# Kernel tuning notes

Hardware: AMD Instinct MI355X
Metric: run time of the kernel (lower is better)

## Reference

```python
import jax, jax.numpy as jnp
import numpy as np

B, N, DIM, QK_DIM, HEADS, GS, M = 4, 8000, 256, 128, 8, 128, 256


def setup_inputs() -> dict:
    key = jax.random.key(0)
    ks = jax.random.split(key, 8)
    normed_x = jax.random.normal(ks[0], (B, N, DIM), jnp.float32)
    # idx_last is a per-batch permutation (token reordering index), shape [B, N, 1]
    idx_last = jax.vmap(lambda k: jax.random.permutation(k, N))(
        jax.random.split(ks[1], B)).astype(jnp.int32)[..., None]
    k_global = jax.random.normal(ks[2], (HEADS, M, QK_DIM // HEADS), jnp.float32)
    v_global = jax.random.normal(ks[3], (HEADS, M, DIM // HEADS), jnp.float32)
    s = 1.0 / np.sqrt(DIM).astype(np.float32)
    Wq = jax.random.normal(ks[4], (QK_DIM, DIM), jnp.float32) * s
    Wk = jax.random.normal(ks[5], (QK_DIM, DIM), jnp.float32) * s
    Wv = jax.random.normal(ks[6], (DIM, DIM), jnp.float32) * s
    Wp = jax.random.normal(ks[7], (DIM, DIM), jnp.float32) * s
    return {"normed_x": normed_x, "idx_last": idx_last, "k_global": k_global,
            "v_global": v_global, "Wq": Wq, "Wk": Wk, "Wv": Wv, "Wp": Wp}


def _forward(normed_x, idx_last, k_global, v_global, Wq, Wk, Wv, Wp):
    x = normed_x
    b, n, _ = x.shape
    h = HEADS
    idx = idx_last[..., 0]  # [B, N]

    q = x @ Wq.T  # [B, N, QK_DIM]
    k = x @ Wk.T  # [B, N, QK_DIM]
    v = x @ Wv.T  # [B, N, DIM]

    # reorder tokens (gather along the token axis)
    q = jnp.take_along_axis(q, idx[:, :, None], axis=1)
    k = jnp.take_along_axis(k, idx[:, :, None], axis=1)
    v = jnp.take_along_axis(v, idx[:, :, None], axis=1)

    gs = min(n, GS)
    ng = (n + gs - 1) // gs
    pad_n = ng * gs - n

    # pad queries by reflecting the tail, then split into ng groups of gs
    pq = jnp.concatenate([q, jnp.flip(q[:, n - pad_n:n], axis=1)], axis=1)
    pq = pq.reshape(b, ng, gs, h, -1).transpose(0, 1, 3, 2, 4)  # b ng h gs dq

    # keys/values padded with an extra gs of reflected tail -> overlapping windows
    kr = jnp.concatenate([k, jnp.flip(k[:, n - pad_n - gs:n], axis=1)], axis=1)
    vr = jnp.concatenate([v, jnp.flip(v[:, n - pad_n - gs:n], axis=1)], axis=1)
    k_win = jnp.concatenate([kr[:, :ng * gs].reshape(b, ng, gs, -1),
                             kr[:, gs:].reshape(b, ng, gs, -1)], axis=2)
    v_win = jnp.concatenate([vr[:, :ng * gs].reshape(b, ng, gs, -1),
                             vr[:, gs:].reshape(b, ng, gs, -1)], axis=2)
    pk = k_win.reshape(b, ng, 2 * gs, h, -1).transpose(0, 1, 3, 2, 4)  # b ng h 2gs dq
    pv = v_win.reshape(b, ng, 2 * gs, h, -1).transpose(0, 1, 3, 2, 4)  # b ng h 2gs dv

    scale = pq.shape[-1] ** (-0.5)

    # local overlapping-window attention
    s1 = jnp.einsum('bghqd,bghkd->bghqk', pq, pk) * scale
    o1 = jnp.einsum('bghqk,bghkd->bghqd', jax.nn.softmax(s1, axis=-1), pv)

    # global attention (k_global/v_global broadcast over batch and groups)
    s2 = jnp.einsum('bghqd,hmd->bghqm', pq, k_global) * scale
    o2 = jnp.einsum('bghqm,hmd->bghqd', jax.nn.softmax(s2, axis=-1), v_global)

    out = (o1 + o2).transpose(0, 1, 3, 2, 4).reshape(b, ng * gs, -1)[:, :n]

    # scatter back to original token order: res[b, idx[b, i]] = out[b, i]
    b_idx = jnp.arange(b)[:, None]
    out = out.at[b_idx, idx].set(out)
    return out @ Wp.T


def reference(normed_x, idx_last, k_global, v_global, Wq, Wk, Wv, Wp):
    return _forward(normed_x, idx_last, k_global, v_global, Wq, Wk, Wv, Wp)
```

## Files before the change

kernel.cpp:

```cpp
#include <hip/hip_runtime.h>

typedef __attribute__((ext_vector_type(8))) short short8;
typedef __attribute__((ext_vector_type(4))) short short4v;
typedef __attribute__((ext_vector_type(4))) float f32x4;
typedef unsigned short ushort_t;

#define MFMA_BF16_K32(A,B,C) __builtin_amdgcn_mfma_f32_16x16x32_bf16(A,B,C,0,0,0)
#define MFMA_BF16_K16(A,B,C) __builtin_amdgcn_mfma_f32_16x16x16bf16_1k(A,B,C,0,0,0)

static constexpr int Bc  = 4;
static constexpr int Nn  = 8000;
static constexpr int N2  = 8192;
static constexpr int DIMc = 256;
static constexpr float SC2 = 0.36067376022224085f;

__device__ __forceinline__ unsigned short f2bf(float f){
  unsigned int u = __float_as_uint(f);
  u = (u + 0x7FFFu + ((u >> 16) & 1u)) >> 16;
  return (unsigned short)u;
}
__device__ __forceinline__ uint2 pack4(f32x4 v){
  uint2 r;
  r.x = (unsigned)f2bf(v[0]) | ((unsigned)f2bf(v[1]) << 16);
  r.y = (unsigned)f2bf(v[2]) | ((unsigned)f2bf(v[3]) << 16);
  return r;
}
__device__ __forceinline__ unsigned cvtpk(float lo, float hi){
  unsigned r;
  asm("v_cvt_pk_bf16_f32 %0, %1, %2" : "=v"(r) : "v"(lo), "v"(hi));
  return r;
}
__device__ __forceinline__ float rexp2(float x){
  float r;
  asm("v_exp_f32 %0, %1" : "=v"(r) : "v"(x));
  return r;
}
__device__ __forceinline__ float bfhi(unsigned u){ return __uint_as_float(u & 0xffff0000u); }
__device__ __forceinline__ float bflo(unsigned u){ return __uint_as_float(u << 16); }
__device__ __forceinline__ int vperm(int t){
  return (t & ~31) | (((t >> 2) & 3) * 8 + ((t >> 4) & 1) * 4 + (t & 3));
}

__global__ __launch_bounds__(256) void prep_kernel(
    const float* __restrict__ Wq, const float* __restrict__ Wk,
    const float* __restrict__ Wv, const float* __restrict__ Wp,
    const float* __restrict__ kg, const float* __restrict__ vg,
    ushort_t* __restrict__ Wc, ushort_t* __restrict__ vgT,
    ushort_t* __restrict__ kgb, ushort_t* __restrict__ Wpb)
{
  int i = blockIdx.x * 256 + threadIdx.x;
  if (i < 131072){
    int r = i >> 8, c = i & 255;
    float v;
    if (r < 128)      v = Wq[r * 256 + c] * SC2;
    else if (r < 256) v = Wk[(r - 128) * 256 + c];
    else              v = Wv[(r - 256) * 256 + c];
    Wc[i] = f2bf(v);
  } else if (i < 196608){
    int j = i - 131072;
    int c = j & 31, m = (j >> 5) & 255, h = j >> 13;
    vgT[(h * 32 + c) * 256 + vperm(m)] = f2bf(vg[j]);
  } else if (i < 229376){
    int j = i - 196608;
    kgb[j] = f2bf(kg[j]);
  } else {
    int j = i - 229376;
    Wpb[j] = f2bf(Wp[j]);
  }
}

__global__ __launch_bounds__(256) void proj_kernel(
    const float* __restrict__ X, const ushort_t* __restrict__ Wc,
    const int* __restrict__ idx, ushort_t* __restrict__ qh,
    ushort_t* __restrict__ kh, ushort_t* __restrict__ vT)
{
  const int b  = blockIdx.y;
  const int r0 = blockIdx.x * 64;
  const int tid = threadIdx.x;
  const int w = tid >> 6, l = tid & 63, g4 = l >> 4, q16 = l & 15;
  __shared__ unsigned Xs[64][132];

  #pragma unroll
  for (int r = 0; r < 16; ++r){
    int row = r * 4 + w;
    int tok = idx[b * Nn + r0 + row];
    float4 xv = reinterpret_cast<const float4*>(X + (size_t)(b * Nn + tok) * DIMc)[l];
    uint2 u; u.x = cvtpk(xv.x, xv.y); u.y = cvtpk(xv.z, xv.w);
    *reinterpret_cast<uint2*>(&Xs[row][l * 2]) = u;
  }
  __syncthreads();

  f32x4 acc[4][8];
  #pragma unroll
  for (int mt = 0; mt < 4; ++mt)
    #pragma unroll
    for (int ct = 0; ct < 8; ++ct) acc[mt][ct] = f32x4{0.f, 0.f, 0.f, 0.f};
  const int colbase = w * 128;
  #pragma unroll
  for (int kc = 0; kc < 8; ++kc){
    short8 a[4];
    #pragma unroll
    for (int mt = 0; mt < 4; ++mt){
      uint4 au = *reinterpret_cast<const uint4*>(&Xs[mt * 16 + q16][kc * 16 + g4 * 4]);
      a[mt] = __builtin_bit_cast(short8, au);
    }
    #pragma unroll
    for (int ct = 0; ct < 8; ++ct){
      int col = colbase + ct * 16 + q16;
      short8 bb = *reinterpret_cast<const short8*>(Wc + col * 256 + kc * 32 + g4 * 8);
      #pragma unroll
      for (int mt = 0; mt < 4; ++mt) acc[mt][ct] = MFMA_BF16_K32(a[mt], bb, acc[mt][ct]);
    }
  }
  if (w < 2){
    ushort_t* dst = (w == 0) ? qh : kh;
    #pragma unroll
    for (int ct = 0; ct < 8; ++ct){
      #pragma unroll
      for (int mt = 0; mt < 4; ++mt){
        #pragma unroll
        for (int r = 0; r < 4; ++r){
          int j = r0 + mt * 16 + g4 * 4 + r;
          dst[((size_t)(b * 8 + ct) * N2 + j) * 16 + q16] = f2bf(acc[mt][ct][r]);
        }
      }
    }
  } else {
    #pragma unroll
    for (int ct = 0; ct < 8; ++ct){
      int col = colbase - 256 + ct * 16 + q16;
      #pragma unroll
      for (int mt = 0; mt < 4; ++mt){
        int jb = r0 + (mt >> 1) * 32 + g4 * 8 + (mt & 1) * 4;
        *reinterpret_cast<uint2*>(vT + (size_t)(b * 256 + col) * N2 + jb) = pack4(acc[mt][ct]);
      }
    }
  }
}

__global__ __launch_bounds__(256) void reflect_fill_kernel(
    ushort_t* __restrict__ qh, ushort_t* __restrict__ kh, ushort_t* __restrict__ vT)
{
  int t = blockIdx.x * 256 + threadIdx.x;
  if (t < 24576){
    int e = t & 1;
    int r = (t >> 1) % 192;
    int p = (t >> 1) / 192;
    int b = p >> 4, q = p & 15;
    ushort_t* base = (q < 8) ? qh : kh;
    int h = q & 7;
    size_t plane = (size_t)(b * 8 + h) * N2 * 16;
    const uint4* src = reinterpret_cast<const uint4*>(base + plane + (size_t)(7999 - r) * 16);
    uint4*       dst = reinterpret_cast<uint4*>(base + plane + (size_t)(8000 + r) * 16);
    dst[e] = src[e];
  } else {
    int u = t - 24576;
    int r = u / 192, i2 = u % 192;
    vT[(size_t)r * N2 + vperm(8000 + i2)] = vT[(size_t)r * N2 + vperm(7999 - i2)];
  }
}

__global__ __launch_bounds__(256) void attn_kernel(
    const ushort_t* __restrict__ qh, const ushort_t* __restrict__ kh,
    const ushort_t* __restrict__ vT,
    const ushort_t* __restrict__ kg, const ushort_t* __restrict__ vgT,
    ushort_t* __restrict__ aoh)
{
  const int go = blockIdx.x, hp = blockIdx.y, b = blockIdx.z;
  const int tid = threadIdx.x;
  const int w = tid >> 6, l = tid & 63, g4 = l >> 4, q16 = l & 15;
  const int h = hp * 4 + w;
  __shared__ unsigned Pex[4][8][16][17];
  const f32x4 z4 = {0.f, 0.f, 0.f, 0.f};
  const size_t bh = (size_t)(b * 8 + h);
  const ushort_t* Kloc = kh + (bh * N2 + go * 128) * 16;
  const ushort_t* Vloc = vT + (size_t)(b * 256 + h * 32) * N2 + go * 128;
  const ushort_t* Kg   = kg + (size_t)h * 256 * 16;
  const ushort_t* Vg   = vgT + (size_t)h * 32 * 256;
  const ushort_t* Qb   = qh + (bh * N2 + go * 128) * 16;
  ushort_t*       Ob   = aoh + (bh * N2 + go * 128) * 32;

  short8 ones;
  #pragma unroll
  for (int j = 0; j < 8; ++j) ones[j] = (short)0x3F80;

  #pragma unroll 1
  for (int pass = 0; pass < 2; ++pass){
    const ushort_t* kbase = (pass == 0) ? Kloc : Kg;
    short4v karr[16];
    #pragma unroll
    for (int t = 0; t < 16; ++t)
      karr[t] = *reinterpret_cast<const short4v*>(
          kbase + (size_t)(t * 16 + q16) * 16 + g4 * 4);
    const ushort_t* v0;
    size_t rstride;
    if (pass == 0){ v0 = Vloc + (size_t)q16 * N2 + g4 * 8;  rstride = (size_t)16 * N2; }
    else          { v0 = Vg   + (size_t)q16 * 256 + g4 * 8; rstride = (size_t)16 * 256; }
    uint4 va[8], vb[8];
    #pragma unroll
    for (int t2 = 0; t2 < 8; ++t2){
      va[t2] = *reinterpret_cast<const uint4*>(v0 + t2 * 32);
      vb[t2] = *reinterpret_cast<const uint4*>(v0 + rstride + t2 * 32);
    }

    #pragma unroll 2
    for (int qt = 0; qt < 8; ++qt){
      short4v qf = *reinterpret_cast<const short4v*>(
          Qb + (size_t)(qt * 16 + q16) * 16 + g4 * 4);
      f32x4 s[16];
      __builtin_amdgcn_s_setprio(1);
      #pragma unroll
      for (int t = 0; t < 16; ++t) s[t] = MFMA_BF16_K16(karr[t], qf, z4);
      __builtin_amdgcn_s_setprio(0);
      uint4 p4[8];
      #pragma unroll
      for (int t2 = 0; t2 < 8; ++t2){
        float e0 = rexp2(s[2*t2][0]);
        float e1 = rexp2(s[2*t2][1]);
        float e2 = rexp2(s[2*t2][2]);
        float e3 = rexp2(s[2*t2][3]);
        float f0 = rexp2(s[2*t2+1][0]);
        float f1 = rexp2(s[2*t2+1][1]);
        float f2 = rexp2(s[2*t2+1][2]);
        float f3 = rexp2(s[2*t2+1][3]);
        p4[t2].x = cvtpk(e0, e1); p4[t2].y = cvtpk(e2, e3);
        p4[t2].z = cvtpk(f0, f1); p4[t2].w = cvtpk(f2, f3);
      }
      f32x4 o0 = z4, o1 = z4, dacc = z4;
      __builtin_amdgcn_s_setprio(1);
      #pragma unroll
      for (int t2 = 0; t2 < 8; ++t2){
        short8 pf = __builtin_bit_cast(short8, p4[t2]);
        o0   = MFMA_BF16_K32(__builtin_bit_cast(short8, va[t2]), pf, o0);
        o1   = MFMA_BF16_K32(__builtin_bit_cast(short8, vb[t2]), pf, o1);
        dacc = MFMA_BF16_K32(ones, pf, dacc);
      }
      __builtin_amdgcn_s_setprio(0);
      float invd = 1.0f / dacc[0];
      unsigned* pb = &Pex[w][qt][q16][0];
      if (pass == 0){
        pb[g4 * 2]         = cvtpk(o0[0] * invd, o0[1] * invd);
        pb[g4 * 2 + 1]     = cvtpk(o0[2] * invd, o0[3] * invd);
        pb[8 + g4 * 2]     = cvtpk(o1[0] * invd, o1[1] * invd);
        pb[8 + g4 * 2 + 1] = cvtpk(o1[2] * invd, o1[3] * invd);
      } else {
        unsigned u0 = pb[g4 * 2],     u1 = pb[g4 * 2 + 1];
        unsigned u2 = pb[8 + g4 * 2], u3 = pb[8 + g4 * 2 + 1];
        f32x4 r0, r1;
        r0[0] = __builtin_fmaf(o0[0], invd, bflo(u0));
        r0[1] = __builtin_fmaf(o0[1], invd, bfhi(u0));
        r0[2] = __builtin_fmaf(o0[2], invd, bflo(u1));
        r0[3] = __builtin_fmaf(o0[3], invd, bfhi(u1));
        r1[0] = __builtin_fmaf(o1[0], invd, bflo(u2));
        r1[1] = __builtin_fmaf(o1[1], invd, bfhi(u2));
        r1[2] = __builtin_fmaf(o1[2], invd, bflo(u3));
        r1[3] = __builtin_fmaf(o1[3], invd, bfhi(u3));
        uint2 s0, s1;
        s0.x = cvtpk(r0[0], r0[1]); s0.y = cvtpk(r0[2], r0[3]);
        s1.x = cvtpk(r1[0], r1[1]); s1.y = cvtpk(r1[2], r1[3]);
        size_t base = (size_t)(qt * 16 + q16) * 32;
        *reinterpret_cast<uint2*>(Ob + base + g4 * 4)      = s0;
        *reinterpret_cast<uint2*>(Ob + base + 16 + g4 * 4) = s1;
      }
    }
  }
}

__global__ __launch_bounds__(256) void final_kernel(
    const ushort_t* __restrict__ A, const ushort_t* __restrict__ Wp,
    const int* __restrict__ idx, float* __restrict__ out)
{
  const int b  = blockIdx.y;
  const int r0 = blockIdx.x * 64;
  const int tid = threadIdx.x;
  const int w = tid >> 6, l = tid & 63, g4 = l >> 4, q16 = l & 15;
  f32x4 acc[4][4];
  #pragma unroll
  for (int mt = 0; mt < 4; ++mt)
    #pragma unroll
    for (int ct = 0; ct < 4; ++ct) acc[mt][ct] = f32x4{0.f, 0.f, 0.f, 0.f};
  const int colbase = w * 64;
  #pragma unroll
  for (int kc = 0; kc < 8; ++kc){
    short8 a[4];
    #pragma unroll
    for (int mt = 0; mt < 4; ++mt)
      a[mt] = *reinterpret_cast<const short8*>(
          A + ((size_t)(b * 8 + kc) * N2 + r0 + mt * 16 + q16) * 32 + g4 * 8);
    #pragma unroll
    for (int ct = 0; ct < 4; ++ct){
      int col = colbase + ct * 16 + q16;
      short8 bb = *reinterpret_cast<const short8*>(Wp + col * 256 + kc * 32 + g4 * 8);
      #pragma unroll
      for (int mt = 0; mt < 4; ++mt) acc[mt][ct] = MFMA_BF16_K32(a[mt], bb, acc[mt][ct]);
    }
  }
  #pragma unroll
  for (int mt = 0; mt < 4; ++mt){
    int orow[4];
    #pragma unroll
    for (int r = 0; r < 4; ++r) orow[r] = idx[b * Nn + r0 + mt * 16 + g4 * 4 + r];
    #pragma unroll
    for (int ct = 0; ct < 4; ++ct){
      int col = colbase + ct * 16 + q16;
      #pragma unroll
      for (int r = 0; r < 4; ++r)
        out[(size_t)(b * Nn + orow[r]) * DIMc + col] = acc[mt][ct][r];
    }
  }
}

extern "C" void kernel_launch(void* const* d_in, const int* in_sizes, int n_in,
                              void* d_out, int out_size, void* d_ws, size_t ws_size,
                              hipStream_t stream)
{
  const float* x   = (const float*)d_in[0];
  const int*   idx = (const int*)d_in[1];
  const float* kg  = (const float*)d_in[2];
  const float* vg  = (const float*)d_in[3];
  const float* Wq  = (const float*)d_in[4];
  const float* Wk  = (const float*)d_in[5];
  const float* Wv  = (const float*)d_in[6];
  const float* Wp  = (const float*)d_in[7];
  float* out = (float*)d_out;

  char* ws = (char*)d_ws;
  size_t off = 0;
  auto alloc = [&](size_t bytes) -> void* {
    void* p = ws + off; off += (bytes + 255) & ~(size_t)255; return p;
  };
  ushort_t* qh   = (ushort_t*)alloc((size_t)Bc * 8 * N2 * 16 * 2);
  ushort_t* kh   = (ushort_t*)alloc((size_t)Bc * 8 * N2 * 16 * 2);
  ushort_t* vT   = (ushort_t*)alloc((size_t)Bc * 256 * N2 * 2);
  ushort_t* aoh  = (ushort_t*)alloc((size_t)Bc * 8 * N2 * 32 * 2);
  ushort_t* Wc   = (ushort_t*)alloc((size_t)512 * 256 * 2);
  ushort_t* vgT  = (ushort_t*)alloc((size_t)8 * 32 * 256 * 2);
  ushort_t* kgb  = (ushort_t*)alloc((size_t)8 * 256 * 16 * 2);
  ushort_t* Wpb  = (ushort_t*)alloc((size_t)256 * 256 * 2);

  hipLaunchKernelGGL(prep_kernel,  dim3(1152), dim3(256), 0, stream,
                     Wq, Wk, Wv, Wp, kg, vg, Wc, vgT, kgb, Wpb);
  hipLaunchKernelGGL(proj_kernel,  dim3(125, 4), dim3(256), 0, stream, x, Wc, idx, qh, kh, vT);
  hipLaunchKernelGGL(reflect_fill_kernel, dim3(864), dim3(256), 0, stream, qh, kh, vT);
  hipLaunchKernelGGL(attn_kernel,  dim3(63, 2, 4), dim3(256), 0, stream, qh, kh, vT, kgb, vgT, aoh);
  hipLaunchKernelGGL(final_kernel, dim3(125, 4), dim3(256), 0, stream, aoh, Wpb, idx, out);
}
```

Before: 100.8 us.

## Pre-swizzle weights and V into MFMA fragment order for coalesced loads

Weights for the projection and output GEMMs are rearranged in the prep kernel into per-lane MFMA fragment order, so each lane loads one contiguous 16-byte chunk. Local and global V are also stored in a fragment-major layout indexed by group, head and lane, which replaces strided transposed reads in the attention kernel with contiguous ones. The goal is to cut uncoalesced global traffic and address arithmetic. In exchange the V stores in the projection and the reflect fill become scattered, with more complex indexing.

```diff
diff --git a/kernel.cpp b/kernel.cpp
--- a/kernel.cpp
+++ b/kernel.cpp
@@ -40,39 +40,54 @@
 __device__ __forceinline__ int vperm(int t){
   return (t & ~31) | (((t >> 2) & 3) * 8 + ((t >> 4) & 1) * 4 + (t & 3));
 }
+__device__ __forceinline__ size_t vf_addr(int b, int p, int h, int half, int q16v){
+  int g = p >> 7, t2 = (p >> 5) & 3, g4 = (p >> 3) & 3, j = p & 7;
+  return ((size_t)((((b * 64 + g) * 8 + h) * 2 + half) * 4 + t2) * 64
+          + g4 * 16 + q16v) * 8 + j;
+}
 
 __global__ __launch_bounds__(256) void prep_kernel(
     const float* __restrict__ Wq, const float* __restrict__ Wk,
     const float* __restrict__ Wv, const float* __restrict__ Wp,
     const float* __restrict__ kg, const float* __restrict__ vg,
-    ushort_t* __restrict__ Wc, ushort_t* __restrict__ vgT,
-    ushort_t* __restrict__ kgb, ushort_t* __restrict__ Wpb)
+    ushort_t* __restrict__ Wcs, ushort_t* __restrict__ Wps,
+    ushort_t* __restrict__ Vgf, ushort_t* __restrict__ kgb)
 {
   int i = blockIdx.x * 256 + threadIdx.x;
   if (i < 131072){
-    int r = i >> 8, c = i & 255;
+    int jj = i & 7, f = i >> 3;
+    int l = f & 63, kc = (f >> 6) & 7, ctw = f >> 9;
+    int col = ctw * 16 + (l & 15);
+    int k   = kc * 32 + (l >> 4) * 8 + jj;
     float v;
-    if (r < 128)      v = Wq[r * 256 + c] * SC2;
-    else if (r < 256) v = Wk[(r - 128) * 256 + c];
-    else              v = Wv[(r - 256) * 256 + c];
-    Wc[i] = f2bf(v);
+    if (col < 128)      v = Wq[col * 256 + k] * SC2;
+    else if (col < 256) v = Wk[(col - 128) * 256 + k];
+    else                v = Wv[(col - 256) * 256 + k];
+    Wcs[i] = f2bf(v);
   } else if (i < 196608){
-    int j = i - 131072;
-    int c = j & 31, m = (j >> 5) & 255, h = j >> 13;
-    vgT[(h * 32 + c) * 256 + vperm(m)] = f2bf(vg[j]);
-  } else if (i < 229376){
-    int j = i - 196608;
+    int o = i - 131072;
+    int jj = o & 7, f = o >> 3;
+    int l = f & 63, kc = (f >> 6) & 7, ctw = f >> 9;
+    int col = ctw * 16 + (l & 15);
+    int k   = kc * 32 + (l >> 4) * 8 + jj;
+    Wps[o] = f2bf(Wp[col * 256 + k]);
+  } else if (i < 262144){
+    int o = i - 196608;
+    int c = o & 31, m = (o >> 5) & 255, h = o >> 13;
+    int p = vperm(m);
+    int t2 = p >> 5, g4 = (p >> 3) & 3, j = p & 7;
+    int half = c >> 4, q16v = c & 15;
+    Vgf[((size_t)((h * 2 + half) * 8 + t2) * 64 + g4 * 16 + q16v) * 8 + j] = f2bf(vg[o]);
+  } else {
+    int j = i - 262144;
     kgb[j] = f2bf(kg[j]);
-  } else {
-    int j = i - 229376;
-    Wpb[j] = f2bf(Wp[j]);
   }
 }
 
 __global__ __launch_bounds__(256) void proj_kernel(
-    const float* __restrict__ X, const ushort_t* __restrict__ Wc,
+    const float* __restrict__ X, const ushort_t* __restrict__ Wcs,
     const int* __restrict__ idx, ushort_t* __restrict__ qh,
-    ushort_t* __restrict__ kh, ushort_t* __restrict__ vT)
+    ushort_t* __restrict__ kh, ushort_t* __restrict__ Vf)
 {
   const int b  = blockIdx.y;
   const int r0 = blockIdx.x * 64;
@@ -95,7 +110,6 @@
   for (int mt = 0; mt < 4; ++mt)
     #pragma unroll
     for (int ct = 0; ct < 8; ++ct) acc[mt][ct] = f32x4{0.f, 0.f, 0.f, 0.f};
-  const int colbase = w * 128;
   #pragma unroll
   for (int kc = 0; kc < 8; ++kc){
     short8 a[4];
@@ -106,8 +120,8 @@
     }
     #pragma unroll
     for (int ct = 0; ct < 8; ++ct){
-      int col = colbase + ct * 16 + q16;
-      short8 bb = *reinterpret_cast<const short8*>(Wc + col * 256 + kc * 32 + g4 * 8);
+      short8 bb = *reinterpret_cast<const short8*>(
+          Wcs + ((size_t)((w * 8 + ct) * 8 + kc) * 64 + l) * 8);
       #pragma unroll
       for (int mt = 0; mt < 4; ++mt) acc[mt][ct] = MFMA_BF16_K32(a[mt], bb, acc[mt][ct]);
     }
@@ -128,18 +142,19 @@
   } else {
     #pragma unroll
     for (int ct = 0; ct < 8; ++ct){
-      int col = colbase - 256 + ct * 16 + q16;
+      int col = (w - 2) * 128 + ct * 16 + q16;
+      int h = col >> 5, dv = col & 31, half = dv >> 4, q16v = dv & 15;
       #pragma unroll
       for (int mt = 0; mt < 4; ++mt){
         int jb = r0 + (mt >> 1) * 32 + g4 * 8 + (mt & 1) * 4;
-        *reinterpret_cast<uint2*>(vT + (size_t)(b * 256 + col) * N2 + jb) = pack4(acc[mt][ct]);
+        *reinterpret_cast<uint2*>(Vf + vf_addr(b, jb, h, half, q16v)) = pack4(acc[mt][ct]);
       }
     }
   }
 }
 
 __global__ __launch_bounds__(256) void reflect_fill_kernel(
-    ushort_t* __restrict__ qh, ushort_t* __restrict__ kh, ushort_t* __restrict__ vT)
+    ushort_t* __restrict__ qh, ushort_t* __restrict__ kh, ushort_t* __restrict__ Vf)
 {
   int t = blockIdx.x * 256 + threadIdx.x;
   if (t < 24576){
@@ -156,14 +171,17 @@
   } else {
     int u = t - 24576;
     int r = u / 192, i2 = u % 192;
-    vT[(size_t)r * N2 + vperm(8000 + i2)] = vT[(size_t)r * N2 + vperm(7999 - i2)];
+    int b = r >> 8, col = r & 255;
+    int h = col >> 5, dv = col & 31, half = dv >> 4, q16v = dv & 15;
+    int pd = vperm(8000 + i2), ps = vperm(7999 - i2);
+    Vf[vf_addr(b, pd, h, half, q16v)] = Vf[vf_addr(b, ps, h, half, q16v)];
   }
 }
 
 __global__ __launch_bounds__(256) void attn_kernel(
     const ushort_t* __restrict__ qh, const ushort_t* __restrict__ kh,
-    const ushort_t* __restrict__ vT,
-    const ushort_t* __restrict__ kg, const ushort_t* __restrict__ vgT,
+    const ushort_t* __restrict__ Vf,
+    const ushort_t* __restrict__ kg, const ushort_t* __restrict__ Vgf,
     ushort_t* __restrict__ aoh)
 {
   const int go = blockIdx.x, hp = blockIdx.y, b = blockIdx.z;
@@ -174,9 +192,7 @@
   const f32x4 z4 = {0.f, 0.f, 0.f, 0.f};
   const size_t bh = (size_t)(b * 8 + h);
   const ushort_t* Kloc = kh + (bh * N2 + go * 128) * 16;
-  const ushort_t* Vloc = vT + (size_t)(b * 256 + h * 32) * N2 + go * 128;
   const ushort_t* Kg   = kg + (size_t)h * 256 * 16;
-  const ushort_t* Vg   = vgT + (size_t)h * 32 * 256;
   const ushort_t* Qb   = qh + (bh * N2 + go * 128) * 16;
   ushort_t*       Ob   = aoh + (bh * N2 + go * 128) * 32;
 
@@ -192,15 +208,24 @@
     for (int t = 0; t < 16; ++t)
       karr[t] = *reinterpret_cast<const short4v*>(
           kbase + (size_t)(t * 16 + q16) * 16 + g4 * 4);
-    const ushort_t* v0;
-    size_t rstride;
-    if (pass == 0){ v0 = Vloc + (size_t)q16 * N2 + g4 * 8;  rstride = (size_t)16 * N2; }
-    else          { v0 = Vg   + (size_t)q16 * 256 + g4 * 8; rstride = (size_t)16 * 256; }
     uint4 va[8], vb[8];
-    #pragma unroll
-    for (int t2 = 0; t2 < 8; ++t2){
-      va[t2] = *reinterpret_cast<const uint4*>(v0 + t2 * 32);
-      vb[t2] = *reinterpret_cast<const uint4*>(v0 + rstride + t2 * 32);
+    if (pass == 0){
+      const ushort_t* g0 = Vf + ((size_t)((b * 64 + go)     * 8 + h) * 2) * 4 * 512;
+      const ushort_t* g1 = Vf + ((size_t)((b * 64 + go + 1) * 8 + h) * 2) * 4 * 512;
+      #pragma unroll
+      for (int t2 = 0; t2 < 8; ++t2){
+        const ushort_t* base = (t2 < 4) ? g0 : g1;
+        int tt = t2 & 3;
+        va[t2] = *reinterpret_cast<const uint4*>(base + (size_t)tt * 512 + l * 8);
+        vb[t2] = *reinterpret_cast<const uint4*>(base + (size_t)(4 + tt) * 512 + l * 8);
+      }
+    } else {
+      const ushort_t* g0 = Vgf + (size_t)(h * 2) * 8 * 512;
+      #pragma unroll
+      for (int t2 = 0; t2 < 8; ++t2){
+        va[t2] = *reinterpret_cast<const uint4*>(g0 + (size_t)t2 * 512 + l * 8);
+        vb[t2] = *reinterpret_cast<const uint4*>(g0 + (size_t)(8 + t2) * 512 + l * 8);
+      }
     }
 
     #pragma unroll 2
@@ -267,7 +292,7 @@
 }
 
 __global__ __launch_bounds__(256) void final_kernel(
-    const ushort_t* __restrict__ A, const ushort_t* __restrict__ Wp,
+    const ushort_t* __restrict__ A, const ushort_t* __restrict__ Wps,
     const int* __restrict__ idx, float* __restrict__ out)
 {
   const int b  = blockIdx.y;
@@ -279,7 +304,6 @@
   for (int mt = 0; mt < 4; ++mt)
     #pragma unroll
     for (int ct = 0; ct < 4; ++ct) acc[mt][ct] = f32x4{0.f, 0.f, 0.f, 0.f};
-  const int colbase = w * 64;
   #pragma unroll
   for (int kc = 0; kc < 8; ++kc){
     short8 a[4];
@@ -289,8 +313,8 @@
           A + ((size_t)(b * 8 + kc) * N2 + r0 + mt * 16 + q16) * 32 + g4 * 8);
     #pragma unroll
     for (int ct = 0; ct < 4; ++ct){
-      int col = colbase + ct * 16 + q16;
-      short8 bb = *reinterpret_cast<const short8*>(Wp + col * 256 + kc * 32 + g4 * 8);
+      short8 bb = *reinterpret_cast<const short8*>(
+          Wps + ((size_t)((w * 4 + ct) * 8 + kc) * 64 + l) * 8);
       #pragma unroll
       for (int mt = 0; mt < 4; ++mt) acc[mt][ct] = MFMA_BF16_K32(a[mt], bb, acc[mt][ct]);
     }
@@ -302,7 +326,7 @@
     for (int r = 0; r < 4; ++r) orow[r] = idx[b * Nn + r0 + mt * 16 + g4 * 4 + r];
     #pragma unroll
     for (int ct = 0; ct < 4; ++ct){
-      int col = colbase + ct * 16 + q16;
+      int col = w * 64 + ct * 16 + q16;
       #pragma unroll
       for (int r = 0; r < 4; ++r)
         out[(size_t)(b * Nn + orow[r]) * DIMc + col] = acc[mt][ct][r];
@@ -331,17 +355,17 @@
   };
   ushort_t* qh   = (ushort_t*)alloc((size_t)Bc * 8 * N2 * 16 * 2);
   ushort_t* kh   = (ushort_t*)alloc((size_t)Bc * 8 * N2 * 16 * 2);
-  ushort_t* vT   = (ushort_t*)alloc((size_t)Bc * 256 * N2 * 2);
+  ushort_t* Vf   = (ushort_t*)alloc((size_t)Bc * 64 * 8 * 2 * 4 * 64 * 8 * 2);
   ushort_t* aoh  = (ushort_t*)alloc((size_t)Bc * 8 * N2 * 32 * 2);
-  ushort_t* Wc   = (ushort_t*)alloc((size_t)512 * 256 * 2);
-  ushort_t* vgT  = (ushort_t*)alloc((size_t)8 * 32 * 256 * 2);
+  ushort_t* Wcs  = (ushort_t*)alloc((size_t)512 * 256 * 2);
+  ushort_t* Wps  = (ushort_t*)alloc((size_t)256 * 256 * 2);
+  ushort_t* Vgf  = (ushort_t*)alloc((size_t)8 * 2 * 8 * 64 * 8 * 2);
   ushort_t* kgb  = (ushort_t*)alloc((size_t)8 * 256 * 16 * 2);
-  ushort_t* Wpb  = (ushort_t*)alloc((size_t)256 * 256 * 2);
 
   hipLaunchKernelGGL(prep_kernel,  dim3(1152), dim3(256), 0, stream,
-                     Wq, Wk, Wv, Wp, kg, vg, Wc, vgT, kgb, Wpb);
-  hipLaunchKernelGGL(proj_kernel,  dim3(125, 4), dim3(256), 0, stream, x, Wc, idx, qh, kh, vT);
-  hipLaunchKernelGGL(reflect_fill_kernel, dim3(864), dim3(256), 0, stream, qh, kh, vT);
-  hipLaunchKernelGGL(attn_kernel,  dim3(63, 2, 4), dim3(256), 0, stream, qh, kh, vT, kgb, vgT, aoh);
-  hipLaunchKernelGGL(final_kernel, dim3(125, 4), dim3(256), 0, stream, aoh, Wpb, idx, out);
-}
+                     Wq, Wk, Wv, Wp, kg, vg, Wcs, Wps, Vgf, kgb);
+  hipLaunchKernelGGL(proj_kernel,  dim3(125, 4), dim3(256), 0, stream, x, Wcs, idx, qh, kh, Vf);
+  hipLaunchKernelGGL(reflect_fill_kernel, dim3(864), dim3(256), 0, stream, qh, kh, Vf);
+  hipLaunchKernelGGL(attn_kernel,  dim3(63, 2, 4), dim3(256), 0, stream, qh, kh, Vf, kgb, Vgf, aoh);
+  hipLaunchKernelGGL(final_kernel, dim3(125, 4), dim3(256), 0, stream, aoh, Wps, idx, out);
+}
```

Measured after the change: 102.9 us. 1.02x slower.
